# Kernel tuning notes

Hardware: AMD Instinct MI355X
Metric: run time of the kernel (lower is better)

Reference implementation:

```python
import jax, jax.numpy as jnp
import numpy as np

B, S, F, O = 128, 8, 32, 16  # batch, board_size, in_features, out_features
D = 2 * S - 1                # diff_size = 15 relative offsets per axis


def setup_inputs() -> dict:
    key = jax.random.key(0)
    k1, k2, k3 = jax.random.split(key, 3)
    inp = jax.random.normal(k1, (B, S, S, F), dtype=jnp.float32)
    # torch.nn.Bilinear init: U(-1/sqrt(in1_features), 1/sqrt(in1_features))
    bound = 1.0 / np.sqrt(F)
    W = jax.random.uniform(k2, (D, D, O, F, F), jnp.float32, -bound, bound)
    b = jax.random.uniform(k3, (D, D, O), jnp.float32, -bound, bound)
    return {"inp": inp, "W": W, "b": b}


def reference(inp, W, b):
    # inp: (B, S, S, F); W: (D, D, O, F, F); b: (D, D, O)
    s = inp.shape[1]
    idx = jnp.arange(s)
    # offset index: off[a, bb] = bb - a + (s - 1), in [0, 2s-2]
    off = idx[None, :] - idx[:, None] + (s - 1)  # (S, S)
    # gather per-pair bilinear weights: Wg[ax, bx, ay, by] = W[bx-ax+7, by-ay+7]
    Wg = W[off[:, :, None, None], off[None, None, :, :]]  # (S,S,S,S,O,F,F)
    bg = b[off[:, :, None, None], off[None, None, :, :]]  # (S,S,S,S,O) [ax,bx,ay,by]
    # out[b, ax, ay, bx, by, o] = a_i W_oij b_j + bias_o
    out = jnp.einsum('bxyi,xXyYoij,bXYj->bxyXYo', inp, Wg, inp)
    out = out + bg.transpose(0, 2, 1, 3, 4)[None]  # bias to [ax,ay,bx,by,o]
    return out
```

## Files before the change

kernel.cpp:

```cpp
#include <hip/hip_runtime.h>

typedef _Float16 f16;
typedef _Float16 f16x8 __attribute__((ext_vector_type(8)));
typedef _Float16 f16x4 __attribute__((ext_vector_type(4)));
typedef float f32x4 __attribute__((ext_vector_type(4)));

#define LDS_OSTRIDE 1032
#define W4 921600
#define I4 65536

__global__ __launch_bounds__(256) void convert_kernel(
    const float* __restrict__ W, const float* __restrict__ inp,
    f16* __restrict__ W_h, f16* __restrict__ inp_h)
{
    const int idx = blockIdx.x * 256 + threadIdx.x;
    if (idx < W4) {
        const float4 v = ((const float4*)W)[idx];
        f16x4 h = { (f16)v.x, (f16)v.y, (f16)v.z, (f16)v.w };
        *(f16x4*)(W_h + (size_t)idx * 4) = h;
    } else {
        const int k = idx - W4;
        const float4 v = ((const float4*)inp)[k];
        f16x4 h = { (f16)v.x, (f16)v.y, (f16)v.z, (f16)v.w };
        *(f16x4*)(inp_h + (size_t)k * 4) = h;
    }
}

template <int HALFSRC>
__global__ __launch_bounds__(256, 4) void rel_mfma(
    const void* __restrict__ Wsrc, const void* __restrict__ isrc,
    const float* __restrict__ bias, float* __restrict__ out)
{
    __shared__ f16 Wl[16 * LDS_OSTRIDE];

    const int bid = blockIdx.x;
    const int Y = bid & 7, X = (bid >> 3) & 7, y = (bid >> 6) & 7, x = (bid >> 9) & 7;
    const int dx = X - x + 7, dy = Y - y + 7;
    const size_t woff = (size_t)(dx * 15 + dy) * 16384;

    const int t = threadIdx.x;

    {
        const int o = t & 15;
        const int r = t >> 4;
        if (HALFSRC) {
            const f16* Wg = (const f16*)Wsrc + woff + o * 1024;
            #pragma unroll
            for (int it = 0; it < 8; ++it) {
                const int within = r + it * 16;
                f16x8 v = *(const f16x8*)(Wg + within * 8);
                *(f16x8*)(&Wl[o * LDS_OSTRIDE + within * 8]) = v;
            }
        } else {
            const float* Wg = (const float*)Wsrc + woff + o * 1024;
            #pragma unroll
            for (int it = 0; it < 8; ++it) {
                const int within = r + it * 16;
                const float4 v0 = *(const float4*)(Wg + within * 8);
                const float4 v1 = *(const float4*)(Wg + within * 8 + 4);
                f16x8 h = { (f16)v0.x, (f16)v0.y, (f16)v0.z, (f16)v0.w,
                            (f16)v1.x, (f16)v1.y, (f16)v1.z, (f16)v1.w };
                *(f16x8*)(&Wl[o * LDS_OSTRIDE + within * 8]) = h;
            }
        }
    }

    const int lane = t & 63;
    const int wave = t >> 6;
    const int quad = lane >> 4;
    const int m = lane & 15;

    f16x8 a0[4], a1[4], c0, c1;
    {
        const int b0 = wave * 32 + m;
        const int b1 = b0 + 16;
        if (HALFSRC) {
            const f16* ih = (const f16*)isrc;
            const f16* ar0 = ih + ((b0 * 8 + x) * 8 + y) * 32;
            const f16* ar1 = ih + ((b1 * 8 + x) * 8 + y) * 32;
            #pragma unroll
            for (int g = 0; g < 4; ++g) {
                a0[g] = *(const f16x8*)(ar0 + g * 8);
                a1[g] = *(const f16x8*)(ar1 + g * 8);
            }
            c0 = *(const f16x8*)(ih + ((b0 * 8 + X) * 8 + Y) * 32 + quad * 8);
            c1 = *(const f16x8*)(ih + ((b1 * 8 + X) * 8 + Y) * 32 + quad * 8);
        } else {
            const float* is = (const float*)isrc;
            const float* ar0 = is + ((b0 * 8 + x) * 8 + y) * 32;
            const float* ar1 = is + ((b1 * 8 + x) * 8 + y) * 32;
            #pragma unroll
            for (int g = 0; g < 4; ++g)
                #pragma unroll
                for (int u = 0; u < 8; ++u) {
                    a0[g][u] = (f16)ar0[g * 8 + u];
                    a1[g][u] = (f16)ar1[g * 8 + u];
                }
            const float* cr0 = is + ((b0 * 8 + X) * 8 + Y) * 32 + quad * 8;
            const float* cr1 = is + ((b1 * 8 + X) * 8 + Y) * 32 + quad * 8;
            #pragma unroll
            for (int u = 0; u < 8; ++u) { c0[u] = (f16)cr0[u]; c1[u] = (f16)cr1[u]; }
        }
    }

    __syncthreads();

    f32x4 acc0 = {0.f, 0.f, 0.f, 0.f};
    f32x4 acc1 = {0.f, 0.f, 0.f, 0.f};
    const f16* wl = &Wl[m * LDS_OSTRIDE + quad * 8];
    #pragma unroll
    for (int g = 0; g < 4; ++g) {
        #pragma unroll
        for (int u = 0; u < 8; ++u) {
            const int kb = g * 8 + u;
            f16x8 bfrag = *(const f16x8*)(wl + kb * 32);
            f16x8 af0 = c0 * a0[g][u];
            f16x8 af1 = c1 * a1[g][u];
            acc0 = __builtin_amdgcn_mfma_f32_16x16x32_f16(af0, bfrag, acc0, 0, 0, 0);
            acc1 = __builtin_amdgcn_mfma_f32_16x16x32_f16(af1, bfrag, acc1, 0, 0, 0);
        }
    }

    const float bv = bias[(dx * 15 + dy) * 16 + m];
    #pragma unroll
    for (int r = 0; r < 4; ++r) {
        const int b0 = wave * 32 + quad * 4 + r;
        const int b1 = b0 + 16;
        out[((size_t)b0 * 4096 + bid) * 16 + m] = acc0[r] + bv;
        out[((size_t)b1 * 4096 + bid) * 16 + m] = acc1[r] + bv;
    }
}

extern "C" void kernel_launch(void* const* d_in, const int* in_sizes, int n_in,
                              void* d_out, int out_size, void* d_ws, size_t ws_size,
                              hipStream_t stream)
{
    const float* inp  = (const float*)d_in[0];
    const float* W    = (const float*)d_in[1];
    const float* bias = (const float*)d_in[2];
    float* out = (float*)d_out;

    const size_t W_H_BYTES   = (size_t)W4 * 4 * sizeof(f16);
    const size_t INP_H_BYTES = (size_t)I4 * 4 * sizeof(f16);

    if (ws_size >= W_H_BYTES + INP_H_BYTES) {
        f16* W_h   = (f16*)d_ws;
        f16* inp_h = (f16*)((char*)d_ws + W_H_BYTES);
        hipLaunchKernelGGL(convert_kernel, dim3((W4 + I4) / 256), dim3(256), 0, stream,
                           W, inp, W_h, inp_h);
        hipLaunchKernelGGL((rel_mfma<1>), dim3(4096), dim3(256), 0, stream,
                           (const void*)W_h, (const void*)inp_h, bias, out);
    } else {
        hipLaunchKernelGGL((rel_mfma<0>), dim3(4096), dim3(256), 0, stream,
                           (const void*)W, (const void*)inp, bias, out);
    }
}
```

Before: 114.7 us.

## Pre-permute fp16 weights for direct global-to-LDS loads and raise occupancy

The conversion kernel now writes the fp16 weights in an [i][o][k] order so each block's 32 KB weight slice is contiguous in MFMA fragment order. The main kernel copies that slice straight into LDS with global_load_lds, with no register staging and no padded stride, and the launch bound asks for 5 blocks per CU instead of 4. The fp32 fallback path is gone, so the workspace is now assumed large enough. Dropping the padding may bring back LDS bank conflicts on the fragment reads.

```diff
diff --git a/kernel.cpp b/kernel.cpp
--- a/kernel.cpp
+++ b/kernel.cpp
@@ -2,66 +2,62 @@
 
 typedef _Float16 f16;
 typedef _Float16 f16x8 __attribute__((ext_vector_type(8)));
-typedef _Float16 f16x4 __attribute__((ext_vector_type(4)));
 typedef float f32x4 __attribute__((ext_vector_type(4)));
+typedef unsigned int u32;
+typedef const __attribute__((address_space(1))) u32* gas1_t;
+typedef __attribute__((address_space(3))) u32* las3_t;
 
-#define LDS_OSTRIDE 1032
-#define W4 921600
-#define I4 65536
+#define WGRAN 460800
+#define IGRAN 32768
 
 __global__ __launch_bounds__(256) void convert_kernel(
     const float* __restrict__ W, const float* __restrict__ inp,
     f16* __restrict__ W_h, f16* __restrict__ inp_h)
 {
-    const int idx = blockIdx.x * 256 + threadIdx.x;
-    if (idx < W4) {
-        const float4 v = ((const float4*)W)[idx];
-        f16x4 h = { (f16)v.x, (f16)v.y, (f16)v.z, (f16)v.w };
-        *(f16x4*)(W_h + (size_t)idx * 4) = h;
+    const int g = blockIdx.x * 256 + threadIdx.x;
+    if (g < WGRAN) {
+        const int dxdy = g >> 11;
+        const int r = g & 2047;
+        const int i = r >> 6, o = (r >> 2) & 15, quad = r & 3;
+        const float* src = W + (size_t)dxdy * 16384 + o * 1024 + i * 32 + quad * 8;
+        const float4 v0 = *(const float4*)src;
+        const float4 v1 = *(const float4*)(src + 4);
+        f16x8 h = { (f16)v0.x, (f16)v0.y, (f16)v0.z, (f16)v0.w,
+                    (f16)v1.x, (f16)v1.y, (f16)v1.z, (f16)v1.w };
+        *(f16x8*)(W_h + (size_t)g * 8) = h;
     } else {
-        const int k = idx - W4;
-        const float4 v = ((const float4*)inp)[k];
-        f16x4 h = { (f16)v.x, (f16)v.y, (f16)v.z, (f16)v.w };
-        *(f16x4*)(inp_h + (size_t)k * 4) = h;
+        const int k = g - WGRAN;
+        const float* src = inp + (size_t)k * 8;
+        const float4 v0 = *(const float4*)src;
+        const float4 v1 = *(const float4*)(src + 4);
+        f16x8 h = { (f16)v0.x, (f16)v0.y, (f16)v0.z, (f16)v0.w,
+                    (f16)v1.x, (f16)v1.y, (f16)v1.z, (f16)v1.w };
+        *(f16x8*)(inp_h + (size_t)k * 8) = h;
     }
 }
 
-template <int HALFSRC>
-__global__ __launch_bounds__(256, 4) void rel_mfma(
-    const void* __restrict__ Wsrc, const void* __restrict__ isrc,
-    const float* __restrict__ bias, float* __restrict__ out)
+__global__ __launch_bounds__(256, 5) void rel_mfma2(
+    const f16* __restrict__ W_h,
+    const f16* __restrict__ inp_h,
+    const float* __restrict__ bias,
+    float* __restrict__ out)
 {
-    __shared__ f16 Wl[16 * LDS_OSTRIDE];
+    __shared__ __align__(16) f16 Wl[16384];
 
     const int bid = blockIdx.x;
     const int Y = bid & 7, X = (bid >> 3) & 7, y = (bid >> 6) & 7, x = (bid >> 9) & 7;
     const int dx = X - x + 7, dy = Y - y + 7;
-    const size_t woff = (size_t)(dx * 15 + dy) * 16384;
+    const int dxdy = dx * 15 + dy;
 
     const int t = threadIdx.x;
 
     {
-        const int o = t & 15;
-        const int r = t >> 4;
-        if (HALFSRC) {
-            const f16* Wg = (const f16*)Wsrc + woff + o * 1024;
-            #pragma unroll
-            for (int it = 0; it < 8; ++it) {
-                const int within = r + it * 16;
-                f16x8 v = *(const f16x8*)(Wg + within * 8);
-                *(f16x8*)(&Wl[o * LDS_OSTRIDE + within * 8]) = v;
-            }
-        } else {
-            const float* Wg = (const float*)Wsrc + woff + o * 1024;
-            #pragma unroll
-            for (int it = 0; it < 8; ++it) {
-                const int within = r + it * 16;
-                const float4 v0 = *(const float4*)(Wg + within * 8);
-                const float4 v1 = *(const float4*)(Wg + within * 8 + 4);
-                f16x8 h = { (f16)v0.x, (f16)v0.y, (f16)v0.z, (f16)v0.w,
-                            (f16)v1.x, (f16)v1.y, (f16)v1.z, (f16)v1.w };
-                *(f16x8*)(&Wl[o * LDS_OSTRIDE + within * 8]) = h;
-            }
+        const f16* base = W_h + (size_t)dxdy * 16384;
+        #pragma unroll
+        for (int it = 0; it < 8; ++it) {
+            const int idx = (it * 256 + t) * 8;
+            __builtin_amdgcn_global_load_lds((gas1_t)(base + idx),
+                                             (las3_t)&Wl[idx], 16, 0, 0);
         }
     }
 
@@ -74,54 +70,36 @@
     {
         const int b0 = wave * 32 + m;
         const int b1 = b0 + 16;
-        if (HALFSRC) {
-            const f16* ih = (const f16*)isrc;
-            const f16* ar0 = ih + ((b0 * 8 + x) * 8 + y) * 32;
-            const f16* ar1 = ih + ((b1 * 8 + x) * 8 + y) * 32;
-            #pragma unroll
-            for (int g = 0; g < 4; ++g) {
-                a0[g] = *(const f16x8*)(ar0 + g * 8);
-                a1[g] = *(const f16x8*)(ar1 + g * 8);
-            }
-            c0 = *(const f16x8*)(ih + ((b0 * 8 + X) * 8 + Y) * 32 + quad * 8);
-            c1 = *(const f16x8*)(ih + ((b1 * 8 + X) * 8 + Y) * 32 + quad * 8);
-        } else {
-            const float* is = (const float*)isrc;
-            const float* ar0 = is + ((b0 * 8 + x) * 8 + y) * 32;
-            const float* ar1 = is + ((b1 * 8 + x) * 8 + y) * 32;
-            #pragma unroll
-            for (int g = 0; g < 4; ++g)
-                #pragma unroll
-                for (int u = 0; u < 8; ++u) {
-                    a0[g][u] = (f16)ar0[g * 8 + u];
-                    a1[g][u] = (f16)ar1[g * 8 + u];
-                }
-            const float* cr0 = is + ((b0 * 8 + X) * 8 + Y) * 32 + quad * 8;
-            const float* cr1 = is + ((b1 * 8 + X) * 8 + Y) * 32 + quad * 8;
-            #pragma unroll
-            for (int u = 0; u < 8; ++u) { c0[u] = (f16)cr0[u]; c1[u] = (f16)cr1[u]; }
+        const f16* ar0 = inp_h + ((b0 * 8 + x) * 8 + y) * 32;
+        const f16* ar1 = inp_h + ((b1 * 8 + x) * 8 + y) * 32;
+        #pragma unroll
+        for (int g = 0; g < 4; ++g) {
+            a0[g] = *(const f16x8*)(ar0 + g * 8);
+            a1[g] = *(const f16x8*)(ar1 + g * 8);
         }
+        c0 = *(const f16x8*)(inp_h + ((b0 * 8 + X) * 8 + Y) * 32 + quad * 8);
+        c1 = *(const f16x8*)(inp_h + ((b1 * 8 + X) * 8 + Y) * 32 + quad * 8);
     }
 
     __syncthreads();
 
     f32x4 acc0 = {0.f, 0.f, 0.f, 0.f};
     f32x4 acc1 = {0.f, 0.f, 0.f, 0.f};
-    const f16* wl = &Wl[m * LDS_OSTRIDE + quad * 8];
+    const f16* wl = &Wl[m * 32 + quad * 8];
     #pragma unroll
     for (int g = 0; g < 4; ++g) {
         #pragma unroll
         for (int u = 0; u < 8; ++u) {
             const int kb = g * 8 + u;
-            f16x8 bfrag = *(const f16x8*)(wl + kb * 32);
-            f16x8 af0 = c0 * a0[g][u];
-            f16x8 af1 = c1 * a1[g][u];
+            const f16x8 bfrag = *(const f16x8*)(wl + kb * 512);
+            const f16x8 af0 = c0 * a0[g][u];
+            const f16x8 af1 = c1 * a1[g][u];
             acc0 = __builtin_amdgcn_mfma_f32_16x16x32_f16(af0, bfrag, acc0, 0, 0, 0);
             acc1 = __builtin_amdgcn_mfma_f32_16x16x32_f16(af1, bfrag, acc1, 0, 0, 0);
         }
     }
 
-    const float bv = bias[(dx * 15 + dy) * 16 + m];
+    const float bv = bias[dxdy * 16 + m];
     #pragma unroll
     for (int r = 0; r < 4; ++r) {
         const int b0 = wave * 32 + quad * 4 + r;
@@ -140,18 +118,11 @@
     const float* bias = (const float*)d_in[2];
     float* out = (float*)d_out;
 
-    const size_t W_H_BYTES   = (size_t)W4 * 4 * sizeof(f16);
-    const size_t INP_H_BYTES = (size_t)I4 * 4 * sizeof(f16);
+    f16* W_h   = (f16*)d_ws;
+    f16* inp_h = (f16*)d_ws + (size_t)WGRAN * 8;
 
-    if (ws_size >= W_H_BYTES + INP_H_BYTES) {
-        f16* W_h   = (f16*)d_ws;
-        f16* inp_h = (f16*)((char*)d_ws + W_H_BYTES);
-        hipLaunchKernelGGL(convert_kernel, dim3((W4 + I4) / 256), dim3(256), 0, stream,
-                           W, inp, W_h, inp_h);
-        hipLaunchKernelGGL((rel_mfma<1>), dim3(4096), dim3(256), 0, stream,
-                           (const void*)W_h, (const void*)inp_h, bias, out);
-    } else {
-        hipLaunchKernelGGL((rel_mfma<0>), dim3(4096), dim3(256), 0, stream,
-                           (const void*)W, (const void*)inp, bias, out);
-    }
+    hipLaunchKernelGGL(convert_kernel, dim3((WGRAN + IGRAN) / 256), dim3(256), 0,
+                       stream, W, inp, W_h, inp_h);
+    hipLaunchKernelGGL(rel_mfma2, dim3(4096), dim3(256), 0, stream,
+                       W_h, inp_h, bias, out);
 }
```

After: 105.9 us. -7.7%, faster.
